# Kernel optimization log

Measured on AMD Instinct MI355X. Metric: run time of the kernel, lower is better.

## Reference

```python
import jax, jax.numpy as jnp
import numpy as np

E = 128  # embedding_dim
C = 32   # per-head dim
H = 4    # heads
L = 256  # seq_len
N = 1    # batch


def layer_norm(x, gamma, beta, eps=1e-5):
    mu = jnp.mean(x, axis=-1, keepdims=True)
    var = jnp.mean((x - mu) ** 2, axis=-1, keepdims=True)
    return (x - mu) * jax.lax.rsqrt(var + eps) * gamma + beta


def setup_inputs() -> dict:
    key = jax.random.key(0)
    ks = jax.random.split(key, 12)
    s = E ** -0.5
    return {
        "pair_rep": jax.random.normal(ks[0], (N, L, L, E), dtype=jnp.float32),
        "mask": jax.random.normal(ks[1], (N, L, L), dtype=jnp.float32) * 0.1,
        "gamma": jnp.ones((E,), dtype=jnp.float32),
        "beta": jnp.zeros((E,), dtype=jnp.float32),
        "Wq": jax.random.normal(ks[2], (E, C * H), dtype=jnp.float32) * s,
        "Wk": jax.random.normal(ks[3], (E, C * H), dtype=jnp.float32) * s,
        "Wv": jax.random.normal(ks[4], (E, C * H), dtype=jnp.float32) * s,
        "Wb": jax.random.normal(ks[5], (E, H), dtype=jnp.float32) * s,
        "Wfu": jax.random.normal(ks[6], (E, C * H), dtype=jnp.float32) * s,
        "bfu": jnp.zeros((C * H,), dtype=jnp.float32),
        "Wo": jax.random.normal(ks[7], (C * H, E), dtype=jnp.float32) * (C * H) ** -0.5,
        "bo": jnp.zeros((E,), dtype=jnp.float32),
    }


def reference(pair_rep, mask, gamma, beta, Wq, Wk, Wv, Wb, Wfu, bfu, Wo, bo):
    n, s, _, _ = pair_rep.shape
    x = layer_norm(pair_rep, gamma, beta)  # [n,s,s,E]
    q = (x @ Wq).reshape(n, s, s, H, C) * (C ** -0.5)
    k = (x @ Wk).reshape(n, s, s, H, C)
    v = (x @ Wv).reshape(n, s, s, H, C)
    # faithful to original einsum: keys carry the q index, queries the v index
    dpa = jnp.einsum('nsqhc,nsvhc->nsqvh', k, q)  # [n,s,q,v,h]
    dpa = dpa + mask[:, None, :, :, None]
    pair_bias = x @ Wb  # [n,s,s,H]
    attn = jax.nn.softmax(dpa + pair_bias[:, None], axis=3)
    out = jnp.einsum('nsqvh,nsvhc->nsqhc', attn, v)  # [n,s,q,h,c]
    fu = jax.nn.sigmoid(x @ Wfu + bfu).reshape(n, s, s, H, C)
    out = out * fu
    out = out.reshape(n, s, s, H * C) @ Wo + bo
    return out
```

## Files before the change

### kernel.cpp

```cpp
#include <hip/hip_runtime.h>
#include <math.h>

#define L 256
#define E 128
#define H 4
#define C 32
#define P (L*L)

typedef __bf16 bf16;
typedef __bf16 bf16x8 __attribute__((ext_vector_type(8)));
typedef __bf16 bf16x4 __attribute__((ext_vector_type(4)));
typedef float  f32x4  __attribute__((ext_vector_type(4)));

#define MFMA(a,b,c) __builtin_amdgcn_mfma_f32_16x16x32_bf16((a),(b),(c),0,0,0)

__global__ __launch_bounds__(256) void k_prep(
    const float* __restrict__ Wq, const float* __restrict__ Wk,
    const float* __restrict__ Wv, const float* __restrict__ Wfu,
    const float* __restrict__ Wo, const float* __restrict__ Wb,
    bf16* __restrict__ WF, bf16* __restrict__ WoF, bf16* __restrict__ WbF)
{
  const int m = blockIdx.x;
  const int lane = threadIdx.x & 63, wv = threadIdx.x >> 6;
  const int g = lane >> 4, l15 = lane & 15;
  if (m < 5) {
    const float* W = (m==0)?Wq:(m==1)?Wk:(m==2)?Wv:(m==3)?Wfu:Wo;
    bf16* dst = (m < 4) ? (WF + (size_t)m * 16384) : WoF;
    const float sc = (m == 0) ? 0.17677669529663689f : 1.0f;
    for (int f = wv; f < 32; f += 4) {
      const int mt = f >> 2, kt = f & 3;
      const int row = 16*mt + l15, k0 = 32*kt + 8*g;
      bf16x8 o;
      #pragma unroll
      for (int j = 0; j < 8; ++j) o[j] = (bf16)(W[(size_t)(k0+j)*128 + row] * sc);
      *(bf16x8*)(dst + ((size_t)f*64 + lane)*8) = o;
    }
  } else {
    const int kt = wv, k0 = 32*kt + 8*g;
    bf16x8 o;
    #pragma unroll
    for (int j = 0; j < 8; ++j)
      o[j] = (l15 < 4) ? (bf16)Wb[(size_t)(k0+j)*4 + l15] : (bf16)0.0f;
    *(bf16x8*)(WbF + ((size_t)kt*64 + lane)*8) = o;
  }
}

__global__ __launch_bounds__(256) void k_ln_proj(
    const float* __restrict__ pr, const float* __restrict__ gamma,
    const float* __restrict__ beta, const float* __restrict__ bfu,
    const bf16* __restrict__ WF, const bf16* __restrict__ WbF,
    bf16* __restrict__ qbh, bf16* __restrict__ kbh, bf16* __restrict__ vbh,
    bf16* __restrict__ gfb, float* __restrict__ pbo)
{
  __shared__ bf16 xs[64 * 136];
  __shared__ bf16 stag[4][16 * 136];
  const int tid = threadIdx.x;
  const int base = blockIdx.x * 64;

  {
    const int pl = tid >> 2, sub = tid & 3;
    const float4* src = (const float4*)(pr + (size_t)(base + pl) * 128 + sub * 32);
    float4 r[8];
    float s = 0.f, ss = 0.f;
    #pragma unroll
    for (int j = 0; j < 8; ++j) {
      r[j] = src[j];
      s  += r[j].x + r[j].y + r[j].z + r[j].w;
      ss += r[j].x*r[j].x + r[j].y*r[j].y + r[j].z*r[j].z + r[j].w*r[j].w;
    }
    s  += __shfl_xor(s, 1, 4);  s  += __shfl_xor(s, 2, 4);
    ss += __shfl_xor(ss, 1, 4); ss += __shfl_xor(ss, 2, 4);
    const float mu   = s * 0.0078125f;
    const float var  = ss * 0.0078125f - mu * mu;
    const float rstd = rsqrtf(var + 1e-5f);
    const float4* g4 = (const float4*)(gamma + sub * 32);
    const float4* b4 = (const float4*)(beta + sub * 32);
    bf16* xr = xs + pl * 136 + sub * 32;
    #pragma unroll
    for (int i = 0; i < 4; ++i) {
      float4 r0 = r[2*i], r1 = r[2*i+1];
      float4 gg0 = g4[2*i], gg1 = g4[2*i+1], bb0 = b4[2*i], bb1 = b4[2*i+1];
      bf16x8 o;
      o[0] = (bf16)((r0.x - mu) * rstd * gg0.x + bb0.x);
      o[1] = (bf16)((r0.y - mu) * rstd * gg0.y + bb0.y);
      o[2] = (bf16)((r0.z - mu) * rstd * gg0.z + bb0.z);
      o[3] = (bf16)((r0.w - mu) * rstd * gg0.w + bb0.w);
      o[4] = (bf16)((r1.x - mu) * rstd * gg1.x + bb1.x);
      o[5] = (bf16)((r1.y - mu) * rstd * gg1.y + bb1.y);
      o[6] = (bf16)((r1.z - mu) * rstd * gg1.z + bb1.z);
      o[7] = (bf16)((r1.w - mu) * rstd * gg1.w + bb1.w);
      *(bf16x8*)(xr + 8 * i) = o;
    }
  }
  __syncthreads();

  const int w = tid >> 6, lane = tid & 63, g = lane >> 4, l15 = lane & 15;
  const f32x4 z = {0.f, 0.f, 0.f, 0.f};

  {
    f32x4 acc = z;
    #pragma unroll
    for (int kt = 0; kt < 4; ++kt) {
      bf16x8 a = *(const bf16x8*)(WbF + ((size_t)kt*64 + lane)*8);
      bf16x8 b = *(const bf16x8*)(xs + (16*w + l15)*136 + 32*kt + 8*g);
      acc = MFMA(a, b, acc);
    }
    if (g == 0)
      *(float4*)(pbo + (size_t)(base + 16*w + l15)*4) =
          make_float4(acc[0], acc[1], acc[2], acc[3]);
  }

  const bf16* WFw = WF + (size_t)w * 16384;
  bf16* stw = stag[w];

  for (int nt = 0; nt < 4; ++nt) {
    bf16x8 bfr[4];
    #pragma unroll
    for (int kt = 0; kt < 4; ++kt)
      bfr[kt] = *(const bf16x8*)(xs + (16*nt + l15)*136 + 32*kt + 8*g);
    f32x4 acc[8];
    #pragma unroll
    for (int mt = 0; mt < 8; ++mt) acc[mt] = z;
    #pragma unroll
    for (int kt = 0; kt < 4; ++kt)
      #pragma unroll
      for (int mt = 0; mt < 8; ++mt) {
        bf16x8 a = *(const bf16x8*)(WFw + ((size_t)(mt*4 + kt)*64 + lane)*8);
        acc[mt] = MFMA(a, bfr[kt], acc[mt]);
      }

    #pragma unroll
    for (int mt = 0; mt < 8; ++mt) {
      const int col = 16*mt + 4*g;
      f32x4 vv = acc[mt];
      if (w == 3) {
        float4 bb = *(const float4*)(bfu + col);
        vv[0] = 1.f / (1.f + __expf(-(vv[0] + bb.x)));
        vv[1] = 1.f / (1.f + __expf(-(vv[1] + bb.y)));
        vv[2] = 1.f / (1.f + __expf(-(vv[2] + bb.z)));
        vv[3] = 1.f / (1.f + __expf(-(vv[3] + bb.w)));
      }
      bf16x4 o;
      o[0] = (bf16)vv[0]; o[1] = (bf16)vv[1]; o[2] = (bf16)vv[2]; o[3] = (bf16)vv[3];
      *(bf16x4*)(stw + l15*136 + col) = o;
    }

    #pragma unroll
    for (int i = 0; i < 4; ++i) {
      const int flat = i*512 + lane*8;
      const int p = flat >> 7, c = flat & 127;
      bf16x8 val = *(const bf16x8*)(stw + p*136 + c);
      if (w == 3) {
        *(bf16x8*)(gfb + ((size_t)(base + 16*nt + p))*128 + c) = val;
      } else {
        bf16* dst = (w == 0) ? qbh : (w == 1) ? kbh : vbh;
        const int h = c >> 5;
        *(bf16x8*)(dst + ((size_t)h*P + base + 16*nt + p)*32 + (c & 31)) = val;
      }
    }
  }
}

__global__ __launch_bounds__(256) void k_bias(
    const float* __restrict__ mask, const float* __restrict__ pb,
    bf16* __restrict__ T4)
{
  const int b = blockIdx.x, h = b >> 4, qt = b & 15;
  const int v = threadIdx.x;
  bf16 row[16];
  #pragma unroll
  for (int q16 = 0; q16 < 16; ++q16) {
    const int q = qt*16 + q16;
    row[q16] = (bf16)(mask[(size_t)q*256 + v] + pb[((size_t)q*256 + v)*4 + h]);
  }
  bf16* dst = T4 + ((size_t)b*256 + v)*16;
  *(bf16x8*)(dst)     = *(bf16x8*)(row);
  *(bf16x8*)(dst + 8) = *(bf16x8*)(row + 8);
}

__global__ __launch_bounds__(256) void k_attn(
    const bf16* __restrict__ qbh, const bf16* __restrict__ kbh,
    const bf16* __restrict__ vbh, const bf16* __restrict__ T4,
    bf16* __restrict__ aob)
{
  __shared__ bf16 qs[256 * 40];
  __shared__ bf16 ps[4][16 * 264];
  const int tid = threadIdx.x;
  const int s = blockIdx.x >> 2, h = blockIdx.x & 3;
  const int rb = s * 256;
  const bf16* qh = qbh + (size_t)h * P * 32;
  const bf16* kh = kbh + (size_t)h * P * 32;
  const bf16* vh = vbh + (size_t)h * P * 32;
  bf16* vT = &ps[0][0];

  #pragma unroll
  for (int i = 0; i < 4; ++i) {
    const int flat = i*2048 + tid*8;
    const int pos = flat >> 5, cc = flat & 31;
    bf16x8 qv = *(const bf16x8*)(qh + ((size_t)rb + pos)*32 + cc);
    *(bf16x8*)(qs + pos*40 + cc) = qv;
    bf16x8 vv = *(const bf16x8*)(vh + ((size_t)rb + pos)*32 + cc);
    #pragma unroll
    for (int j = 0; j < 8; ++j) vT[(cc + j)*264 + pos] = vv[j];
  }
  __syncthreads();

  const int w = tid >> 6, lane = tid & 63, g = lane >> 4, l15 = lane & 15;

  bf16x8 av[2][8];
  #pragma unroll
  for (int mt = 0; mt < 2; ++mt)
    #pragma unroll
    for (int kt = 0; kt < 8; ++kt)
      av[mt][kt] = *(const bf16x8*)(vT + (16*mt + l15)*264 + 32*kt + 8*g);
  __syncthreads();

  bf16* psw = ps[w];
  const bf16* T4h = T4 + (size_t)h * 16 * 4096;
  bf16* aoh = aob + (size_t)h * P * 32;
  const f32x4 z = {0.f, 0.f, 0.f, 0.f};

  for (int qt = 0; qt < 4; ++qt) {
    const int q0 = w*64 + qt*16;

    const bf16* Tsl = T4h + (size_t)(q0 >> 4) * 4096;
    #pragma unroll
    for (int i = 0; i < 8; ++i) {
      const int flat = i*512 + lane*8;
      *(bf16x8*)(psw + flat) = *(const bf16x8*)(Tsl + flat);
    }

    bf16x8 ak = *(const bf16x8*)(kh + ((size_t)rb + q0 + l15)*32 + 8*g);
    f32x4 sc[16];
    #pragma unroll
    for (int t = 0; t < 16; ++t) {
      bf16x8 bq = *(const bf16x8*)(qs + (16*t + l15)*40 + 8*g);
      sc[t] = MFMA(ak, bq, z);
    }

    float rs0 = 0.f, rs1 = 0.f, rs2 = 0.f, rs3 = 0.f;
    #pragma unroll
    for (int t = 0; t < 16; ++t) {
      bf16x4 bb = *(const bf16x4*)(psw + (16*t + l15)*16 + 4*g);
      float e0 = __expf(sc[t][0] + (float)bb[0]); sc[t][0] = e0; rs0 += e0;
      float e1 = __expf(sc[t][1] + (float)bb[1]); sc[t][1] = e1; rs1 += e1;
      float e2 = __expf(sc[t][2] + (float)bb[2]); sc[t][2] = e2; rs2 += e2;
      float e3 = __expf(sc[t][3] + (float)bb[3]); sc[t][3] = e3; rs3 += e3;
    }
    #pragma unroll
    for (int m = 1; m < 16; m <<= 1) {
      rs0 += __shfl_xor(rs0, m, 16);
      rs1 += __shfl_xor(rs1, m, 16);
      rs2 += __shfl_xor(rs2, m, 16);
      rs3 += __shfl_xor(rs3, m, 16);
    }
    const float i0 = 1.f/rs0, i1 = 1.f/rs1, i2 = 1.f/rs2, i3 = 1.f/rs3;

    #pragma unroll
    for (int t = 0; t < 16; ++t) {
      const int vcol = 16*t + l15;
      psw[(4*g + 0)*264 + vcol] = (bf16)(sc[t][0] * i0);
      psw[(4*g + 1)*264 + vcol] = (bf16)(sc[t][1] * i1);
      psw[(4*g + 2)*264 + vcol] = (bf16)(sc[t][2] * i2);
      psw[(4*g + 3)*264 + vcol] = (bf16)(sc[t][3] * i3);
    }

    f32x4 o0 = z, o1 = z;
    #pragma unroll
    for (int kt = 0; kt < 8; ++kt) {
      bf16x8 bp = *(const bf16x8*)(psw + l15*264 + 32*kt + 8*g);
      o0 = MFMA(av[0][kt], bp, o0);
      o1 = MFMA(av[1][kt], bp, o1);
    }
    bf16x4 p0, p1;
    p0[0] = (bf16)o0[0]; p0[1] = (bf16)o0[1]; p0[2] = (bf16)o0[2]; p0[3] = (bf16)o0[3];
    p1[0] = (bf16)o1[0]; p1[1] = (bf16)o1[1]; p1[2] = (bf16)o1[2]; p1[3] = (bf16)o1[3];
    bf16* dst = aoh + ((size_t)rb + q0 + l15)*32;
    *(bf16x4*)(dst + 4*g)      = p0;
    *(bf16x4*)(dst + 16 + 4*g) = p1;
  }
}

__global__ __launch_bounds__(256) void k_gate_out(
    const bf16* __restrict__ aob, const bf16* __restrict__ gfb,
    const bf16* __restrict__ WoF, const float* __restrict__ bo,
    float* __restrict__ out)
{
  __shared__ bf16 gs[64 * 136];
  const int tid = threadIdx.x;
  const int base = blockIdx.x * 64;

  #pragma unroll
  for (int i = 0; i < 4; ++i) {
    const int flat = i*2048 + tid*8;
    const int pos = flat >> 7, c = flat & 127, h = c >> 5;
    bf16x8 a = *(const bf16x8*)(aob + ((size_t)h*P + base + pos)*32 + (c & 31));
    bf16x8 f = *(const bf16x8*)(gfb + ((size_t)(base + pos))*128 + c);
    bf16x8 o;
    #pragma unroll
    for (int j = 0; j < 8; ++j) o[j] = (bf16)((float)a[j] * (float)f[j]);
    *(bf16x8*)(gs + pos*136 + c) = o;
  }
  __syncthreads();

  const int w = tid >> 6, lane = tid & 63, g = lane >> 4, l15 = lane & 15;
  const f32x4 z = {0.f, 0.f, 0.f, 0.f};

  for (int nt = 0; nt < 4; ++nt) {
    bf16x8 bfr[4];
    #pragma unroll
    for (int kt = 0; kt < 4; ++kt)
      bfr[kt] = *(const bf16x8*)(gs + (16*nt + l15)*136 + 32*kt + 8*g);
    f32x4 a0 = z, a1 = z;
    #pragma unroll
    for (int kt = 0; kt < 4; ++kt) {
      bf16x8 af0 = *(const bf16x8*)(WoF + ((size_t)((2*w+0)*4 + kt)*64 + lane)*8);
      bf16x8 af1 = *(const bf16x8*)(WoF + ((size_t)((2*w+1)*4 + kt)*64 + lane)*8);
      a0 = MFMA(af0, bfr[kt], a0);
      a1 = MFMA(af1, bfr[kt], a1);
    }
    const int pos = base + 16*nt + l15;
    {
      const int col = 16*(2*w + 0) + 4*g;
      float4 bb = *(const float4*)(bo + col);
      *(float4*)(out + (size_t)pos*128 + col) =
          make_float4(a0[0] + bb.x, a0[1] + bb.y, a0[2] + bb.z, a0[3] + bb.w);
    }
    {
      const int col = 16*(2*w + 1) + 4*g;
      float4 bb = *(const float4*)(bo + col);
      *(float4*)(out + (size_t)pos*128 + col) =
          make_float4(a1[0] + bb.x, a1[1] + bb.y, a1[2] + bb.z, a1[3] + bb.w);
    }
  }
}

extern "C" void kernel_launch(void* const* d_in, const int* in_sizes, int n_in,
                              void* d_out, int out_size, void* d_ws, size_t ws_size,
                              hipStream_t stream) {
  const float* pr    = (const float*)d_in[0];
  const float* mask  = (const float*)d_in[1];
  const float* gamma = (const float*)d_in[2];
  const float* beta  = (const float*)d_in[3];
  const float* Wq    = (const float*)d_in[4];
  const float* Wk    = (const float*)d_in[5];
  const float* Wv    = (const float*)d_in[6];
  const float* Wb    = (const float*)d_in[7];
  const float* Wfu   = (const float*)d_in[8];
  const float* bfu   = (const float*)d_in[9];
  const float* Wo    = (const float*)d_in[10];
  const float* bo    = (const float*)d_in[11];
  float* out = (float*)d_out;

  bf16* qbh = (bf16*)d_ws;
  bf16* kbh = qbh + (size_t)H * P * 32;
  bf16* vbh = kbh + (size_t)H * P * 32;
  bf16* gfb = vbh + (size_t)H * P * 32;
  bf16* aob = gfb + (size_t)P * 128;
  bf16* T4  = aob + (size_t)H * P * 32;
  bf16* WF  = T4  + (size_t)H * P;
  bf16* WoF = WF  + 4 * 16384;
  bf16* WbF = WoF + 16384;
  float* pb = (float*)(WbF + 2048);

  k_prep<<<6, 256, 0, stream>>>(Wq, Wk, Wv, Wfu, Wo, Wb, WF, WoF, WbF);
  k_ln_proj<<<1024, 256, 0, stream>>>(pr, gamma, beta, bfu, WF, WbF,
                                      qbh, kbh, vbh, gfb, pb);
  k_bias<<<64, 256, 0, stream>>>(mask, pb, T4);
  k_attn<<<1024, 256, 0, stream>>>(qbh, kbh, vbh, T4, aob);
  k_gate_out<<<1024, 256, 0, stream>>>(aob, gfb, WoF, bo, out);
}
```

Before: 203.1 us.

## Keep softmax probabilities in registers by transposing score MFMA and swizzling LDS

Attention now computes the transposed score tile (queries as the A operand, key row as B), so the exp'd probabilities come straight out of the accumulator in the layout the P·V MFMA needs. This removes the LDS round trip for probabilities and the per-wave bias staging. Normalisation is deferred until after the P·V product. The Q tile rows are permuted and the V transpose is XOR-swizzled to avoid bank conflicts. The bias kernel now writes a plain [h][q][v] layout read directly from global memory. The exp is done without max subtraction, and the row sum is accumulated from bf16-rounded values.

```diff
diff --git a/kernel.cpp b/kernel.cpp
--- a/kernel.cpp
+++ b/kernel.cpp
@@ -163,45 +163,47 @@
 
 __global__ __launch_bounds__(256) void k_bias(
     const float* __restrict__ mask, const float* __restrict__ pb,
-    bf16* __restrict__ T4)
-{
-  const int b = blockIdx.x, h = b >> 4, qt = b & 15;
+    bf16* __restrict__ T5)
+{
+  const int q = blockIdx.x;
   const int v = threadIdx.x;
-  bf16 row[16];
-  #pragma unroll
-  for (int q16 = 0; q16 < 16; ++q16) {
-    const int q = qt*16 + q16;
-    row[q16] = (bf16)(mask[(size_t)q*256 + v] + pb[((size_t)q*256 + v)*4 + h]);
-  }
-  bf16* dst = T4 + ((size_t)b*256 + v)*16;
-  *(bf16x8*)(dst)     = *(bf16x8*)(row);
-  *(bf16x8*)(dst + 8) = *(bf16x8*)(row + 8);
+  const size_t qv = (size_t)q*256 + v;
+  const float m = mask[qv];
+  float4 p = *(const float4*)(pb + qv*4);
+  T5[qv]            = (bf16)(m + p.x);
+  T5[qv +   65536]  = (bf16)(m + p.y);
+  T5[qv + 2*65536]  = (bf16)(m + p.z);
+  T5[qv + 3*65536]  = (bf16)(m + p.w);
 }
 
 __global__ __launch_bounds__(256) void k_attn(
     const bf16* __restrict__ qbh, const bf16* __restrict__ kbh,
-    const bf16* __restrict__ vbh, const bf16* __restrict__ T4,
+    const bf16* __restrict__ vbh, const bf16* __restrict__ T5,
     bf16* __restrict__ aob)
 {
   __shared__ bf16 qs[256 * 40];
-  __shared__ bf16 ps[4][16 * 264];
+  __shared__ bf16 vT[32 * 264];
   const int tid = threadIdx.x;
   const int s = blockIdx.x >> 2, h = blockIdx.x & 3;
   const int rb = s * 256;
   const bf16* qh = qbh + (size_t)h * P * 32;
   const bf16* kh = kbh + (size_t)h * P * 32;
   const bf16* vh = vbh + (size_t)h * P * 32;
-  bf16* vT = &ps[0][0];
+  const bf16* T5h = T5 + (size_t)h * 65536;
 
   #pragma unroll
   for (int i = 0; i < 4; ++i) {
     const int flat = i*2048 + tid*8;
     const int pos = flat >> 5, cc = flat & 31;
+    const int slot = (pos & 0xE3) | ((pos & 0x04) << 2) | ((pos & 0x18) >> 1);
     bf16x8 qv = *(const bf16x8*)(qh + ((size_t)rb + pos)*32 + cc);
-    *(bf16x8*)(qs + pos*40 + cc) = qv;
+    *(bf16x8*)(qs + slot*40 + cc) = qv;
     bf16x8 vv = *(const bf16x8*)(vh + ((size_t)rb + pos)*32 + cc);
     #pragma unroll
-    for (int j = 0; j < 8; ++j) vT[(cc + j)*264 + pos] = vv[j];
+    for (int j = 0; j < 8; ++j) {
+      const int row = cc + j;
+      vT[row*264 + (pos ^ ((row >> 3) << 5))] = vv[j];
+    }
   }
   __syncthreads();
 
@@ -209,73 +211,53 @@
 
   bf16x8 av[2][8];
   #pragma unroll
-  for (int mt = 0; mt < 2; ++mt)
+  for (int mt = 0; mt < 2; ++mt) {
+    const int row = 16*mt + l15;
+    const int X = (row >> 3) << 5;
     #pragma unroll
     for (int kt = 0; kt < 8; ++kt)
-      av[mt][kt] = *(const bf16x8*)(vT + (16*mt + l15)*264 + 32*kt + 8*g);
-  __syncthreads();
-
-  bf16* psw = ps[w];
-  const bf16* T4h = T4 + (size_t)h * 16 * 4096;
+      av[mt][kt] = *(const bf16x8*)(vT + row*264 + ((32*kt + 8*g) ^ X));
+  }
+
   bf16* aoh = aob + (size_t)h * P * 32;
   const f32x4 z = {0.f, 0.f, 0.f, 0.f};
 
   for (int qt = 0; qt < 4; ++qt) {
-    const int q0 = w*64 + qt*16;
-
-    const bf16* Tsl = T4h + (size_t)(q0 >> 4) * 4096;
-    #pragma unroll
-    for (int i = 0; i < 8; ++i) {
-      const int flat = i*512 + lane*8;
-      *(bf16x8*)(psw + flat) = *(const bf16x8*)(Tsl + flat);
-    }
-
-    bf16x8 ak = *(const bf16x8*)(kh + ((size_t)rb + q0 + l15)*32 + 8*g);
-    f32x4 sc[16];
-    #pragma unroll
-    for (int t = 0; t < 16; ++t) {
-      bf16x8 bq = *(const bf16x8*)(qs + (16*t + l15)*40 + 8*g);
-      sc[t] = MFMA(ak, bq, z);
-    }
-
-    float rs0 = 0.f, rs1 = 0.f, rs2 = 0.f, rs3 = 0.f;
-    #pragma unroll
-    for (int t = 0; t < 16; ++t) {
-      bf16x4 bb = *(const bf16x4*)(psw + (16*t + l15)*16 + 4*g);
-      float e0 = __expf(sc[t][0] + (float)bb[0]); sc[t][0] = e0; rs0 += e0;
-      float e1 = __expf(sc[t][1] + (float)bb[1]); sc[t][1] = e1; rs1 += e1;
-      float e2 = __expf(sc[t][2] + (float)bb[2]); sc[t][2] = e2; rs2 += e2;
-      float e3 = __expf(sc[t][3] + (float)bb[3]); sc[t][3] = e3; rs3 += e3;
-    }
-    #pragma unroll
-    for (int m = 1; m < 16; m <<= 1) {
-      rs0 += __shfl_xor(rs0, m, 16);
-      rs1 += __shfl_xor(rs1, m, 16);
-      rs2 += __shfl_xor(rs2, m, 16);
-      rs3 += __shfl_xor(rs3, m, 16);
-    }
-    const float i0 = 1.f/rs0, i1 = 1.f/rs1, i2 = 1.f/rs2, i3 = 1.f/rs3;
-
-    #pragma unroll
-    for (int t = 0; t < 16; ++t) {
-      const int vcol = 16*t + l15;
-      psw[(4*g + 0)*264 + vcol] = (bf16)(sc[t][0] * i0);
-      psw[(4*g + 1)*264 + vcol] = (bf16)(sc[t][1] * i1);
-      psw[(4*g + 2)*264 + vcol] = (bf16)(sc[t][2] * i2);
-      psw[(4*g + 3)*264 + vcol] = (bf16)(sc[t][3] * i3);
-    }
-
+    const int q = w*64 + qt*16 + l15;
+    bf16x8 bq = *(const bf16x8*)(kh + ((size_t)rb + q)*32 + 8*g);
+    const bf16* Trow = T5h + (size_t)q * 256 + 8*g;
     f32x4 o0 = z, o1 = z;
+    float rs = 0.f;
     #pragma unroll
     for (int kt = 0; kt < 8; ++kt) {
-      bf16x8 bp = *(const bf16x8*)(psw + l15*264 + 32*kt + 8*g);
-      o0 = MFMA(av[0][kt], bp, o0);
-      o1 = MFMA(av[1][kt], bp, o1);
-    }
+      bf16x8 a0 = *(const bf16x8*)(qs + (16*(2*kt + 0) + l15)*40 + 8*g);
+      bf16x8 a1 = *(const bf16x8*)(qs + (16*(2*kt + 1) + l15)*40 + 8*g);
+      f32x4 s0 = MFMA(a0, bq, z);
+      f32x4 s1 = MFMA(a1, bq, z);
+      bf16x4 b0 = *(const bf16x4*)(Trow + 32*kt);
+      bf16x4 b1 = *(const bf16x4*)(Trow + 32*kt + 4);
+      bf16x8 pf;
+      #pragma unroll
+      for (int r = 0; r < 4; ++r) {
+        float e0 = __expf(s0[r] + (float)b0[r]);
+        float e1 = __expf(s1[r] + (float)b1[r]);
+        pf[r]     = (bf16)e0;
+        pf[4 + r] = (bf16)e1;
+        rs += (float)pf[r] + (float)pf[4 + r];
+      }
+      o0 = MFMA(av[0][kt], pf, o0);
+      o1 = MFMA(av[1][kt], pf, o1);
+    }
+    rs += __shfl_xor(rs, 16);
+    rs += __shfl_xor(rs, 32);
+    const float inv = 1.f / rs;
     bf16x4 p0, p1;
-    p0[0] = (bf16)o0[0]; p0[1] = (bf16)o0[1]; p0[2] = (bf16)o0[2]; p0[3] = (bf16)o0[3];
-    p1[0] = (bf16)o1[0]; p1[1] = (bf16)o1[1]; p1[2] = (bf16)o1[2]; p1[3] = (bf16)o1[3];
-    bf16* dst = aoh + ((size_t)rb + q0 + l15)*32;
+    #pragma unroll
+    for (int r = 0; r < 4; ++r) {
+      p0[r] = (bf16)(o0[r] * inv);
+      p1[r] = (bf16)(o1[r] * inv);
+    }
+    bf16* dst = aoh + ((size_t)rb + q)*32;
     *(bf16x4*)(dst + 4*g)      = p0;
     *(bf16x4*)(dst + 16 + 4*g) = p1;
   }
@@ -357,8 +339,8 @@
   bf16* vbh = kbh + (size_t)H * P * 32;
   bf16* gfb = vbh + (size_t)H * P * 32;
   bf16* aob = gfb + (size_t)P * 128;
-  bf16* T4  = aob + (size_t)H * P * 32;
-  bf16* WF  = T4  + (size_t)H * P;
+  bf16* T5  = aob + (size_t)H * P * 32;
+  bf16* WF  = T5  + (size_t)H * P;
   bf16* WoF = WF  + 4 * 16384;
   bf16* WbF = WoF + 16384;
   float* pb = (float*)(WbF + 2048);
@@ -366,7 +348,7 @@
   k_prep<<<6, 256, 0, stream>>>(Wq, Wk, Wv, Wfu, Wo, Wb, WF, WoF, WbF);
   k_ln_proj<<<1024, 256, 0, stream>>>(pr, gamma, beta, bfu, WF, WbF,
                                       qbh, kbh, vbh, gfb, pb);
-  k_bias<<<64, 256, 0, stream>>>(mask, pb, T4);
-  k_attn<<<1024, 256, 0, stream>>>(qbh, kbh, vbh, T4, aob);
+  k_bias<<<256, 256, 0, stream>>>(mask, pb, T5);
+  k_attn<<<1024, 256, 0, stream>>>(qbh, kbh, vbh, T5, aob);
   k_gate_out<<<1024, 256, 0, stream>>>(aob, gfb, WoF, bo, out);
 }
```

Result: faster. 187.0 us (-7.9%).
